# Optimization experiments

Hardware: AMD Instinct MI355X
Metric: run time of the kernel (lower is better)

The kernel has to match this reference:

```python
import jax, jax.numpy as jnp
import numpy as np

H = 1024

def _cell(xt, h, c, Wi, bi, Wh, bh):
    # gates: [B, 4H], torch Linear is x @ W.T + b; gate order i,f,g,o
    gates = xt @ Wi.T + bi + h @ Wh.T + bh
    i, f, g, o = jnp.split(gates, 4, axis=1)
    i = jax.nn.sigmoid(i)
    f = jax.nn.sigmoid(f)
    g = jnp.tanh(g)
    o = jax.nn.sigmoid(o)
    c_next = f * c + i * g
    h_next = o * jnp.tanh(c_next)
    return h_next, c_next

def setup_inputs() -> dict:
    key = jax.random.key(0)
    ks = jax.random.split(key, 12)
    vocab, E, out_dim = 32000, 1024, 32000
    B, T = 32, 512
    std = 1.0 / np.sqrt(H)
    u = lambda k, shape: jax.random.uniform(k, shape, jnp.float32, -std, std)
    return {
        "x": jax.random.randint(ks[0], (B, T), 0, vocab, dtype=jnp.int32),
        "emb": jax.random.normal(ks[1], (vocab, E), jnp.float32),
        "Wi0": u(ks[2], (4 * H, E)),  "bi0": u(ks[3], (4 * H,)),
        "Wh0": u(ks[4], (4 * H, H)), "bh0": u(ks[5], (4 * H,)),
        "Wi1": u(ks[6], (4 * H, H)), "bi1": u(ks[7], (4 * H,)),
        "Wh1": u(ks[8], (4 * H, H)), "bh1": u(ks[9], (4 * H,)),
        "fc_w": u(ks[10], (out_dim, H)) * (std * np.sqrt(H)) / np.sqrt(H),
        "fc_b": u(ks[11], (out_dim,)),
    }

def reference(x, emb, Wi0, bi0, Wh0, bh0, Wi1, bi1, Wh1, bh1, fc_w, fc_b):
    B, T = x.shape
    xe = emb[x]  # [B, T, E]
    xe = jnp.transpose(xe, (1, 0, 2))  # [T, B, E]
    init = (jnp.zeros((B, H), xe.dtype), jnp.zeros((B, H), xe.dtype),
            jnp.zeros((B, H), xe.dtype), jnp.zeros((B, H), xe.dtype))

    def step(carry, xt):
        h0, c0, h1, c1 = carry
        h0, c0 = _cell(xt, h0, c0, Wi0, bi0, Wh0, bh0)
        h1, c1 = _cell(h0, h1, c1, Wi1, bi1, Wh1, bh1)
        return (h0, c0, h1, c1), None

    (h0, c0, h1, c1), _ = jax.lax.scan(step, init, xe)
    return h1 @ fc_w.T + fc_b  # [B, out_dim]
```

## Files before the change

kernel.cpp:

```cpp
#include <hip/hip_runtime.h>
#include <hip/hip_bf16.h>

typedef __attribute__((ext_vector_type(8))) short short8;
typedef __attribute__((ext_vector_type(4))) float f32x4;
typedef unsigned short u16;
typedef unsigned int u32;
typedef unsigned long long u64;

#define MFMA_BF16(a, b, c) __builtin_amdgcn_mfma_f32_16x16x32_bf16((a), (b), (c), 0, 0, 0)

static constexpr size_t OFF_W   = 0;
static constexpr size_t OFF_B0  = 33554432;
static constexpr size_t OFF_B1  = OFF_B0 + 16384;
static constexpr size_t OFF_H0  = OFF_B1 + 16384;
static constexpr size_t OFF_H1F = OFF_H0 + 262144;
static constexpr size_t OFF_XE  = OFF_H1F + 131072;
static constexpr size_t OFF_X0  = OFF_XE + 33554432;
static constexpr size_t WS_NEED = OFF_X0 + 134217728;
static constexpr size_t OFF_FLG = OFF_X0 - 32768;


__device__ __forceinline__ u16 f2bf(float f) {
  u32 x = __builtin_bit_cast(u32, f);
  x += 0x7fffu + ((x >> 16) & 1u);
  return (u16)(x >> 16);
}
__device__ __forceinline__ float bf2f(u16 u) {
  return __builtin_bit_cast(float, (u32)u << 16);
}
__device__ __forceinline__ float sigm(float x) { return 1.f / (1.f + expf(-x)); }

__device__ __forceinline__ void sysstore64(void* p, u64 v) {
  __hip_atomic_store((u64*)p, v, __ATOMIC_RELAXED, __HIP_MEMORY_SCOPE_SYSTEM);
}
__device__ __forceinline__ u16 sysload16(const u16* p) {
  return __hip_atomic_load(p, __ATOMIC_RELAXED, __HIP_MEMORY_SCOPE_SYSTEM);
}

__device__ __forceinline__ void gload_lds16(const u16* gsrc, u16* ldst) {
  __builtin_amdgcn_global_load_lds(
      (__attribute__((address_space(1))) void*)(u16*)gsrc,
      (__attribute__((address_space(3))) void*)ldst, 16, 0, 0);
}

__global__ void prep_w_kernel(const float* __restrict__ Wi0, const float* __restrict__ Wh0,
                              const float* __restrict__ Wi1, const float* __restrict__ Wh1,
                              u16* __restrict__ dst) {
  size_t e = ((size_t)blockIdx.x * 256 + threadIdx.x) * 4;
  int mat = (int)(e >> 22);
  size_t off = e & ((1ull << 22) - 1);
  const float* src = (mat == 0) ? Wi0 : (mat == 1) ? Wh0 : (mat == 2) ? Wi1 : Wh1;
  float4 v = *(const float4*)(src + off);
  ushort4 o;
  o.x = f2bf(v.x); o.y = f2bf(v.y); o.z = f2bf(v.z); o.w = f2bf(v.w);
  *(ushort4*)(dst + e) = o;
}

__global__ void prep_b_kernel(const float* __restrict__ bi0, const float* __restrict__ bh0,
                              const float* __restrict__ bi1, const float* __restrict__ bh1,
                              float* __restrict__ b0, float* __restrict__ b1) {
  int i = blockIdx.x * 256 + threadIdx.x;
  b0[i] = bi0[i] + bh0[i];
  b1[i] = bi1[i] + bh1[i];
}

__global__ void embed_kernel(const int* __restrict__ x, const float* __restrict__ emb,
                             u16* __restrict__ xe) {
  int m = blockIdx.x;
  int b = m & 31, t = m >> 5;
  int id = x[b * 512 + t];
  float4 v = ((const float4*)(emb + (size_t)id * 1024))[threadIdx.x];
  ushort4 o;
  o.x = f2bf(v.x); o.y = f2bf(v.y); o.z = f2bf(v.z); o.w = f2bf(v.w);
  *(ushort4*)(xe + (size_t)m * 1024 + threadIdx.x * 4) = o;
}

__global__ void x0_gemm_kernel(const u16* __restrict__ A, const u16* __restrict__ W,
                               const float* __restrict__ bias, u16* __restrict__ C) {
  __shared__ u16 lds[2][2][8192];
  const int tid = threadIdx.x, l = tid & 63, w = tid >> 6;
  const int n0 = blockIdx.x * 128, m0 = blockIdx.y * 128;
  const int wm = w >> 1, wn = w & 1;
  const int row8 = l >> 3, u = l & 7;

  f32x4 acc[4][4];
#pragma unroll
  for (int a1 = 0; a1 < 4; ++a1)
#pragma unroll
    for (int a2 = 0; a2 < 4; ++a2) acc[a1][a2] = (f32x4){0.f, 0.f, 0.f, 0.f};

  auto stage = [&](int buf, int kt) {
    const int k0 = kt * 64;
#pragma unroll
    for (int q = 0; q < 4; ++q) {
      const int ld = w * 4 + q;
      const int row = ld * 8 + row8;
      const int sw = (u ^ (row & 7)) * 8;
      gload_lds16(A + (size_t)(m0 + row) * 1024 + k0 + sw, &lds[buf][0][ld * 512]);
      gload_lds16(W + (size_t)(n0 + row) * 1024 + k0 + sw, &lds[buf][1][ld * 512]);
    }
  };

  stage(0, 0);
  __syncthreads();

  for (int kt = 0; kt < 16; ++kt) {
    const int buf = kt & 1;
    if (kt < 15) stage(buf ^ 1, kt + 1);
    const u16* la = lds[buf][0];
    const u16* lb = lds[buf][1];
#pragma unroll
    for (int kk = 0; kk < 2; ++kk) {
      const int c = kk * 4 + (l >> 4);
      const int csw = (c ^ (l & 7)) * 8;
      short8 af[4], bf[4];
#pragma unroll
      for (int mi = 0; mi < 4; ++mi) {
        int row = wm * 64 + mi * 16 + (l & 15);
        af[mi] = *(const short8*)(la + row * 64 + csw);
      }
#pragma unroll
      for (int ni = 0; ni < 4; ++ni) {
        int row = wn * 64 + ni * 16 + (l & 15);
        bf[ni] = *(const short8*)(lb + row * 64 + csw);
      }
#pragma unroll
      for (int mi = 0; mi < 4; ++mi)
#pragma unroll
        for (int ni = 0; ni < 4; ++ni)
          acc[mi][ni] = MFMA_BF16(af[mi], bf[ni], acc[mi][ni]);
    }
    __syncthreads();
  }

#pragma unroll
  for (int ni = 0; ni < 4; ++ni) {
    int col = n0 + wn * 64 + ni * 16 + (l & 15);
    float bv = bias[col];
#pragma unroll
    for (int mi = 0; mi < 4; ++mi) {
#pragma unroll
      for (int r = 0; r < 4; ++r) {
        int row = m0 + wm * 64 + mi * 16 + (l >> 4) * 4 + r;
        C[(size_t)row * 4096 + col] = f2bf(acc[mi][ni][r] + bv);
      }
    }
  }
}

__launch_bounds__(256, 1)
__global__ void lstm_kernel(const u16* __restrict__ wbf, const float* __restrict__ b1v,
                            const u16* __restrict__ X0, u16* __restrict__ hinit,
                            float* __restrict__ h1f, u32* __restrict__ flags) {
  extern __shared__ char smem[];
  u16* wlds = (u16*)smem;
  float* gates0 = (float*)(smem + 98304);
  float* part1  = (float*)(smem + 98304 + 2048);
  float* wh1p   = (float*)(smem + 98304 + 4096);

  const int tid = threadIdx.x;
  const int l = tid & 63, w = tid >> 6;
  const int blk = blockIdx.x;
  const int hbase = blk * 4;
  u16* X0w = (u16*)X0;

  for (int m = 0; m < 3; ++m) {
    const u16* Wm = wbf + (size_t)(m + 1) * (4096 * 1024);
    for (int s = tid; s < 2048; s += 256) {
      int kk = s >> 6, ll = s & 63;
      int nl = ll & 15, hi = ll >> 4;
      int gr = (nl >> 2) * 1024 + hbase + (nl & 3);
      short8 v = *(const short8*)(Wm + (size_t)gr * 1024 + kk * 32 + hi * 8);
      *(short8*)(wlds + m * 16384 + kk * 512 + ll * 8) = v;
    }
  }
  __syncthreads();

  float cst = 0.f;
  const int at = tid & 127, ab = at >> 2, aj = at & 3;
  const int mt = w & 1;

  float b1i = 0.f, b1fv = 0.f, b1g = 0.f, b1o = 0.f;
  if (tid >= 128) {
    b1i  = b1v[hbase + aj];
    b1fv = b1v[1024 + hbase + aj];
    b1g  = b1v[2048 + hbase + aj];
    b1o  = b1v[3072 + hbase + aj];
  }

  const u32* myflag = flags + (size_t)tid * 32;
  u32* ownflag = flags + (size_t)blk * 32;

  for (int i = 0; i <= 512; ++i) {
    const u16* slot_r = (i == 0) ? hinit
                      : (i == 1) ? hinit + 65536
                                 : X0 + (size_t)(i - 2) * 131072;
    u16* slot_w = (i == 0) ? hinit + 65536
                           : X0w + (size_t)(i - 1) * 131072;

    asm volatile("" ::: "memory");

    float xg0 = 0.f, xg1 = 0.f, xg2 = 0.f, xg3 = 0.f;
    if (tid < 128 && i < 512) {
      const u16* xp = X0 + (size_t)(i * 32 + ab) * 4096 + hbase + aj;
      xg0 = bf2f(sysload16(xp));
      xg1 = bf2f(sysload16(xp + 1024));
      xg2 = bf2f(sysload16(xp + 2048));
      xg3 = bf2f(sysload16(xp + 3072));
    }

    const u16* abase = slot_r + (w < 2 ? 0 : 32768)
                     + (mt * 16 + (l & 15)) * 1024 + ((l >> 4) * 8);
    short8 ar[32];
#pragma unroll
    for (int kk = 0; kk < 32; ++kk)
      ar[kk] = *(const short8*)(abase + kk * 32);

    if (w < 2) {
      f32x4 a0a = {0,0,0,0}, a0b = {0,0,0,0}, a1a = {0,0,0,0}, a1b = {0,0,0,0};
#pragma unroll
      for (int kk = 0; kk < 16; ++kk) {
        a0a = MFMA_BF16(ar[2 * kk],     *(const short8*)(wlds + (2 * kk) * 512 + l * 8), a0a);
        a1a = MFMA_BF16(ar[2 * kk],     *(const short8*)(wlds + 16384 + (2 * kk) * 512 + l * 8), a1a);
        a0b = MFMA_BF16(ar[2 * kk + 1], *(const short8*)(wlds + (2 * kk + 1) * 512 + l * 8), a0b);
        a1b = MFMA_BF16(ar[2 * kk + 1], *(const short8*)(wlds + 16384 + (2 * kk + 1) * 512 + l * 8), a1b);
      }
#pragma unroll
      for (int r = 0; r < 4; ++r) {
        int row = mt * 16 + (l >> 4) * 4 + r, col = l & 15;
        gates0[row * 16 + col] = a0a[r] + a0b[r];
        part1[row * 16 + col]  = a1a[r] + a1b[r];
      }
    } else {
      f32x4 a0a = {0,0,0,0}, a0b = {0,0,0,0};
#pragma unroll
      for (int kk = 0; kk < 16; ++kk) {
        a0a = MFMA_BF16(ar[2 * kk],     *(const short8*)(wlds + 2 * 16384 + (2 * kk) * 512 + l * 8), a0a);
        a0b = MFMA_BF16(ar[2 * kk + 1], *(const short8*)(wlds + 2 * 16384 + (2 * kk + 1) * 512 + l * 8), a0b);
      }
#pragma unroll
      for (int r = 0; r < 4; ++r) {
        int row = mt * 16 + (l >> 4) * 4 + r, col = l & 15;
        wh1p[row * 16 + col] = a0a[r] + a0b[r];
      }
    }
    __syncthreads();

    if (tid < 128) {
      if (i < 512) {
        float gi = gates0[ab * 16 + aj]      + xg0;
        float gf = gates0[ab * 16 + 4 + aj]  + xg1;
        float gg = gates0[ab * 16 + 8 + aj]  + xg2;
        float go = gates0[ab * 16 + 12 + aj] + xg3;
        cst = sigm(gf) * cst + sigm(gi) * tanhf(gg);
        float h = sigm(go) * tanhf(cst);
        u32 hv = (u32)f2bf(h);
        u32 p1 = (u32)__shfl_xor((int)hv, 1);
        u32 lo = (aj & 1) ? ((p1 & 0xffff) | (hv << 16)) : ((hv & 0xffff) | (p1 << 16));
        u32 p2 = (u32)__shfl_xor((int)lo, 2);
        if (aj == 0)
          sysstore64(slot_w + ab * 1024 + hbase, (u64)lo | ((u64)p2 << 32));
      }
    } else {
      if (i >= 1) {
        float gi = part1[ab * 16 + aj]      + wh1p[ab * 16 + aj]      + b1i;
        float gf = part1[ab * 16 + 4 + aj]  + wh1p[ab * 16 + 4 + aj]  + b1fv;
        float gg = part1[ab * 16 + 8 + aj]  + wh1p[ab * 16 + 8 + aj]  + b1g;
        float go = part1[ab * 16 + 12 + aj] + wh1p[ab * 16 + 12 + aj] + b1o;
        cst = sigm(gf) * cst + sigm(gi) * tanhf(gg);
        float h = sigm(go) * tanhf(cst);
        u32 hv = (u32)f2bf(h);
        u32 p1 = (u32)__shfl_xor((int)hv, 1);
        u32 lo = (aj & 1) ? ((p1 & 0xffff) | (hv << 16)) : ((hv & 0xffff) | (p1 << 16));
        u32 p2 = (u32)__shfl_xor((int)lo, 2);
        if (aj == 0)
          sysstore64(slot_w + 32768 + ab * 1024 + hbase, (u64)lo | ((u64)p2 << 32));
        if (i == 512) h1f[ab * 1024 + hbase + aj] = h;
      }
    }

    __syncthreads();
    const u32 target = (u32)(i + 1);
    if (tid == 0)
      __hip_atomic_store(ownflag, target, __ATOMIC_RELAXED, __HIP_MEMORY_SCOPE_SYSTEM);
    while (__hip_atomic_load(myflag, __ATOMIC_RELAXED, __HIP_MEMORY_SCOPE_SYSTEM) < target)
      __builtin_amdgcn_s_sleep(1);
    __syncthreads();
  }
}

__global__ void fc_kernel(const float* __restrict__ h1f, const float* __restrict__ fcw,
                          const float* __restrict__ fcb, float* __restrict__ out) {
  int gid = blockIdx.x * 256 + threadIdx.x;
  int v = gid >> 5, b = gid & 31;
  const float4* wr = (const float4*)(fcw + (size_t)v * 1024);
  const float4* hr = (const float4*)(h1f + (size_t)b * 1024);
  float s = 0.f;
#pragma unroll 8
  for (int i = 0; i < 256; ++i) {
    float4 wv = wr[i], hv = hr[i];
    s += wv.x * hv.x + wv.y * hv.y + wv.z * hv.z + wv.w * hv.w;
  }
  out[(size_t)b * 32000 + v] = s + fcb[v];
}

extern "C" void kernel_launch(void* const* d_in, const int* in_sizes, int n_in,
                              void* d_out, int out_size, void* d_ws, size_t ws_size,
                              hipStream_t stream) {
  const int*   x   = (const int*)d_in[0];
  const float* emb = (const float*)d_in[1];
  const float* Wi0 = (const float*)d_in[2];
  const float* bi0 = (const float*)d_in[3];
  const float* Wh0 = (const float*)d_in[4];
  const float* bh0 = (const float*)d_in[5];
  const float* Wi1 = (const float*)d_in[6];
  const float* bi1 = (const float*)d_in[7];
  const float* Wh1 = (const float*)d_in[8];
  const float* bh1 = (const float*)d_in[9];
  const float* fcw = (const float*)d_in[10];
  const float* fcb = (const float*)d_in[11];
  float* out = (float*)d_out;
  char* ws = (char*)d_ws;

  if (ws_size < WS_NEED) return;

  u16*   wbf = (u16*)(ws + OFF_W);
  float* b0v = (float*)(ws + OFF_B0);
  float* b1v = (float*)(ws + OFF_B1);
  u16*   hin = (u16*)(ws + OFF_H0);
  float* h1f = (float*)(ws + OFF_H1F);
  u16*   xe  = (u16*)(ws + OFF_XE);
  u16*   X0p = (u16*)(ws + OFF_X0);
  u32*   flg = (u32*)(ws + OFF_FLG);

  hipMemsetAsync(ws + OFF_H0, 0, OFF_XE - OFF_H0, stream);

  prep_w_kernel<<<16384, 256, 0, stream>>>(Wi0, Wh0, Wi1, Wh1, wbf);
  prep_b_kernel<<<16, 256, 0, stream>>>(bi0, bh0, bi1, bh1, b0v, b1v);
  embed_kernel<<<16384, 256, 0, stream>>>(x, emb, xe);
  x0_gemm_kernel<<<dim3(32, 128), 256, 0, stream>>>(xe, wbf, b0v, X0p);

  hipMemsetAsync(ws + OFF_FLG, 0, 32768, stream);

  hipFuncSetAttribute((const void*)lstm_kernel,
                      hipFuncAttributeMaxDynamicSharedMemorySize, 104448);
  lstm_kernel<<<256, 256, 104448, stream>>>(wbf, b1v, X0p, hin, h1f, flg);

  fc_kernel<<<4000, 256, 0, stream>>>(h1f, fcw, fcb, out);
}
```

Before: 4.098 ms.

## Pack flags densely, poll with one wave, and prefetch repacked input gates

Per-block flags move from one flag per 128-byte line to a dense array, and a single wave polls them with dwordx4 cache-bypassing loads plus a wave-wide all-check, replacing every thread spinning on its own flag. The x0 GEMM output is re-laid out so each thread's four gate values for its block are contiguous, letting one 64-bit load replace four 16-bit system loads. That load is issued for the next step before the barrier wait, hiding its latency. Dense flags may add cache-line contention between writers, and the layout change couples the GEMM epilogue to the LSTM's indexing.

```diff
diff --git a/kernel.cpp b/kernel.cpp
--- a/kernel.cpp
+++ b/kernel.cpp
@@ -3,6 +3,7 @@
 
 typedef __attribute__((ext_vector_type(8))) short short8;
 typedef __attribute__((ext_vector_type(4))) float f32x4;
+typedef __attribute__((ext_vector_type(4))) int i32x4;
 typedef unsigned short u16;
 typedef unsigned int u32;
 typedef unsigned long long u64;
@@ -17,7 +18,7 @@
 static constexpr size_t OFF_XE  = OFF_H1F + 131072;
 static constexpr size_t OFF_X0  = OFF_XE + 33554432;
 static constexpr size_t WS_NEED = OFF_X0 + 134217728;
-static constexpr size_t OFF_FLG = OFF_X0 - 32768;
+static constexpr size_t OFF_FLG = OFF_X0 - 4096;
 
 
 __device__ __forceinline__ u16 f2bf(float f) {
@@ -33,8 +34,8 @@
 __device__ __forceinline__ void sysstore64(void* p, u64 v) {
   __hip_atomic_store((u64*)p, v, __ATOMIC_RELAXED, __HIP_MEMORY_SCOPE_SYSTEM);
 }
-__device__ __forceinline__ u16 sysload16(const u16* p) {
-  return __hip_atomic_load(p, __ATOMIC_RELAXED, __HIP_MEMORY_SCOPE_SYSTEM);
+__device__ __forceinline__ u64 sysload64(const void* p) {
+  return __hip_atomic_load((const u64*)p, __ATOMIC_RELAXED, __HIP_MEMORY_SCOPE_SYSTEM);
 }
 
 __device__ __forceinline__ void gload_lds16(const u16* gsrc, u16* ldst) {
@@ -76,7 +77,7 @@
 }
 
 __global__ void x0_gemm_kernel(const u16* __restrict__ A, const u16* __restrict__ W,
-                               const float* __restrict__ bias, u16* __restrict__ C) {
+                               const float* __restrict__ bias, u16* __restrict__ Xp) {
   __shared__ u16 lds[2][2][8192];
   const int tid = threadIdx.x, l = tid & 63, w = tid >> 6;
   const int n0 = blockIdx.x * 128, m0 = blockIdx.y * 128;
@@ -136,13 +137,16 @@
 #pragma unroll
   for (int ni = 0; ni < 4; ++ni) {
     int col = n0 + wn * 64 + ni * 16 + (l & 15);
+    int g = col >> 10, blkid = (col & 1023) >> 2, j = col & 3;
     float bv = bias[col];
 #pragma unroll
     for (int mi = 0; mi < 4; ++mi) {
 #pragma unroll
       for (int r = 0; r < 4; ++r) {
         int row = m0 + wm * 64 + mi * 16 + (l >> 4) * 4 + r;
-        C[(size_t)row * 4096 + col] = f2bf(acc[mi][ni][r] + bv);
+        int t = row >> 5, b = row & 31;
+        Xp[(size_t)t * 131072 + blkid * 512 + b * 16 + j * 4 + g] =
+            f2bf(acc[mi][ni][r] + bv);
       }
     }
   }
@@ -150,8 +154,8 @@
 
 __launch_bounds__(256, 1)
 __global__ void lstm_kernel(const u16* __restrict__ wbf, const float* __restrict__ b1v,
-                            const u16* __restrict__ X0, u16* __restrict__ hinit,
-                            float* __restrict__ h1f, u32* __restrict__ flags) {
+                            const u16* __restrict__ Xp, u16* __restrict__ hinit,
+                            float* __restrict__ h1f, u32* __restrict__ flagsD) {
   extern __shared__ char smem[];
   u16* wlds = (u16*)smem;
   float* gates0 = (float*)(smem + 98304);
@@ -162,7 +166,7 @@
   const int l = tid & 63, w = tid >> 6;
   const int blk = blockIdx.x;
   const int hbase = blk * 4;
-  u16* X0w = (u16*)X0;
+  u16* Xw = (u16*)Xp;
 
   for (int m = 0; m < 3; ++m) {
     const u16* Wm = wbf + (size_t)(m + 1) * (4096 * 1024);
@@ -188,26 +192,20 @@
     b1o  = b1v[3072 + hbase + aj];
   }
 
-  const u32* myflag = flags + (size_t)tid * 32;
-  u32* ownflag = flags + (size_t)blk * 32;
+  u64 gchunk = 0;
+  if (tid < 128)
+    gchunk = sysload64(Xp + blk * 512 + ab * 16 + aj * 4);
+
+  const u32* fquad = flagsD + l * 4;
 
   for (int i = 0; i <= 512; ++i) {
     const u16* slot_r = (i == 0) ? hinit
                       : (i == 1) ? hinit + 65536
-                                 : X0 + (size_t)(i - 2) * 131072;
+                                 : Xp + (size_t)(i - 2) * 131072;
     u16* slot_w = (i == 0) ? hinit + 65536
-                           : X0w + (size_t)(i - 1) * 131072;
+                           : Xw + (size_t)(i - 1) * 131072;
 
     asm volatile("" ::: "memory");
-
-    float xg0 = 0.f, xg1 = 0.f, xg2 = 0.f, xg3 = 0.f;
-    if (tid < 128 && i < 512) {
-      const u16* xp = X0 + (size_t)(i * 32 + ab) * 4096 + hbase + aj;
-      xg0 = bf2f(sysload16(xp));
-      xg1 = bf2f(sysload16(xp + 1024));
-      xg2 = bf2f(sysload16(xp + 2048));
-      xg3 = bf2f(sysload16(xp + 3072));
-    }
 
     const u16* abase = slot_r + (w < 2 ? 0 : 32768)
                      + (mt * 16 + (l & 15)) * 1024 + ((l >> 4) * 8);
@@ -248,10 +246,10 @@
 
     if (tid < 128) {
       if (i < 512) {
-        float gi = gates0[ab * 16 + aj]      + xg0;
-        float gf = gates0[ab * 16 + 4 + aj]  + xg1;
-        float gg = gates0[ab * 16 + 8 + aj]  + xg2;
-        float go = gates0[ab * 16 + 12 + aj] + xg3;
+        float gi = gates0[ab * 16 + aj]      + bf2f((u16)(gchunk));
+        float gf = gates0[ab * 16 + 4 + aj]  + bf2f((u16)(gchunk >> 16));
+        float gg = gates0[ab * 16 + 8 + aj]  + bf2f((u16)(gchunk >> 32));
+        float go = gates0[ab * 16 + 12 + aj] + bf2f((u16)(gchunk >> 48));
         cst = sigm(gf) * cst + sigm(gi) * tanhf(gg);
         float h = sigm(go) * tanhf(cst);
         u32 hv = (u32)f2bf(h);
@@ -279,12 +277,27 @@
       }
     }
 
+    if (i == 512) break;
+
     __syncthreads();
     const u32 target = (u32)(i + 1);
     if (tid == 0)
-      __hip_atomic_store(ownflag, target, __ATOMIC_RELAXED, __HIP_MEMORY_SCOPE_SYSTEM);
-    while (__hip_atomic_load(myflag, __ATOMIC_RELAXED, __HIP_MEMORY_SCOPE_SYSTEM) < target)
-      __builtin_amdgcn_s_sleep(1);
+      __hip_atomic_store(&flagsD[blk], target, __ATOMIC_RELAXED, __HIP_MEMORY_SCOPE_SYSTEM);
+
+    if (tid < 128 && i + 1 < 512)
+      gchunk = sysload64(Xp + (size_t)(i + 1) * 131072 + blk * 512 + ab * 16 + aj * 4);
+
+    if (w == 0) {
+      while (true) {
+        i32x4 v;
+        asm volatile("global_load_dwordx4 %0, %1, off sc0 sc1"
+                     : "=&v"(v) : "v"(fquad));
+        asm volatile("s_waitcnt vmcnt(0)" ::: "memory");
+        u32 m01 = min((u32)v.x, (u32)v.y);
+        u32 m23 = min((u32)v.z, (u32)v.w);
+        if (__all(min(m01, m23) >= target)) break;
+      }
+    }
     __syncthreads();
   }
 }
@@ -330,7 +343,7 @@
   u16*   hin = (u16*)(ws + OFF_H0);
   float* h1f = (float*)(ws + OFF_H1F);
   u16*   xe  = (u16*)(ws + OFF_XE);
-  u16*   X0p = (u16*)(ws + OFF_X0);
+  u16*   Xp  = (u16*)(ws + OFF_X0);
   u32*   flg = (u32*)(ws + OFF_FLG);
 
   hipMemsetAsync(ws + OFF_H0, 0, OFF_XE - OFF_H0, stream);
@@ -338,13 +351,13 @@
   prep_w_kernel<<<16384, 256, 0, stream>>>(Wi0, Wh0, Wi1, Wh1, wbf);
   prep_b_kernel<<<16, 256, 0, stream>>>(bi0, bh0, bi1, bh1, b0v, b1v);
   embed_kernel<<<16384, 256, 0, stream>>>(x, emb, xe);
-  x0_gemm_kernel<<<dim3(32, 128), 256, 0, stream>>>(xe, wbf, b0v, X0p);
-
-  hipMemsetAsync(ws + OFF_FLG, 0, 32768, stream);
+  x0_gemm_kernel<<<dim3(32, 128), 256, 0, stream>>>(xe, wbf, b0v, Xp);
+
+  hipMemsetAsync(ws + OFF_FLG, 0, 4096, stream);
 
   hipFuncSetAttribute((const void*)lstm_kernel,
                       hipFuncAttributeMaxDynamicSharedMemorySize, 104448);
-  lstm_kernel<<<256, 256, 104448, stream>>>(wbf, b1v, X0p, hin, h1f, flg);
+  lstm_kernel<<<256, 256, 104448, stream>>>(wbf, b1v, Xp, hin, h1f, flg);
 
   fc_kernel<<<4000, 256, 0, stream>>>(h1f, fcw, fcb, out);
 }
```

Result: faster. 3.805 ms (-7.1%).
